# Performance work log

Hardware: AMD Instinct MI355X
Metric: run time of the kernel (lower is better)

## Reference

```python
import jax, jax.numpy as jnp
import numpy as np

N_NODES = 10000
N_EDGES = 320000
D_IN = 128
D_HID = 256
D_OUT = 128


def setup_inputs() -> dict:
    key = jax.random.key(0)
    k = jax.random.split(key, 6)
    idx_i = jax.random.randint(k[0], (N_EDGES,), 0, N_NODES)
    idx_j = jax.random.randint(k[1], (N_EDGES,), 0, N_NODES)
    prop = jax.random.normal(k[2], (N_NODES, D_IN), dtype=jnp.float32)
    basis = jax.random.normal(k[3], (N_EDGES, D_IN), dtype=jnp.float32)
    W1 = jax.random.normal(k[4], (D_IN, D_HID), dtype=jnp.float32) * (1.0 / np.sqrt(D_IN))
    b1 = jnp.zeros((D_HID,), dtype=jnp.float32)
    W2 = jax.random.normal(k[5], (D_HID, D_OUT), dtype=jnp.float32) * (1.0 / np.sqrt(D_HID))
    b2 = jnp.zeros((D_OUT,), dtype=jnp.float32)
    return {"idx_i": idx_i, "idx_j": idx_j, "prop": prop, "basis": basis,
            "W1": W1, "b1": b1, "W2": W2, "b2": b2}


def reference(idx_i, idx_j, prop, basis, W1, b1, W2, b2):
    # gather node features to edges, combine with basis: [E, D_IN]
    inter = prop[idx_i] + basis + prop[idx_j]
    # MLP: Linear(128->256) + tanh, then Linear(256->128) (no final activation)
    h = jnp.tanh(inter @ W1 + b1)  # [E, D_HID]
    out = h @ W2 + b2              # [E, D_OUT]
    return out
```

## Files before the change

kernel.cpp:

```cpp
#include <hip/hip_runtime.h>


#define N_EDGES 320000
#define DI 128
#define DH 256
#define DO 128
#define TM 64

typedef _Float16 half8v __attribute__((ext_vector_type(8)));
typedef _Float16 half4v __attribute__((ext_vector_type(4)));
typedef float floatx16 __attribute__((ext_vector_type(16)));

__device__ __forceinline__ float fast_tanh(float x) {
    float ax = __builtin_fabsf(x);
    float e = __expf(2.0f * ax);
    float t = 1.0f - 2.0f * __builtin_amdgcn_rcpf(e + 1.0f);
    return __builtin_copysignf(t, x);
}

__global__ __launch_bounds__(256) void wconvert(
    const float* __restrict__ W1, const float* __restrict__ W2,
    _Float16* __restrict__ W1T, _Float16* __restrict__ W2T)
{
    __shared__ float sT[32][33];
    int b = blockIdx.x;
    const float* src; _Float16* dst; int R, C, r0, c0;
    if (b < 32) { src = W1; dst = W1T; R = DI;  C = DH; r0 = (b & 3) * 32;  c0 = (b >> 2) * 32; }
    else { b -= 32; src = W2; dst = W2T; R = DH; C = DO; r0 = (b & 7) * 32; c0 = (b >> 3) * 32; }

    const int tid = threadIdx.x;
    const int cc = tid & 31, rr = tid >> 5;
    #pragma unroll
    for (int p = 0; p < 4; ++p) {
        int r = rr + p * 8;
        sT[r][cc] = src[(size_t)(r0 + r) * C + c0 + cc];
    }
    __syncthreads();
    #pragma unroll
    for (int p = 0; p < 4; ++p) {
        int c = rr + p * 8;
        dst[(size_t)(c0 + c) * R + r0 + cc] = (_Float16)sT[cc][c];
    }
}

__global__ __launch_bounds__(256) void pilayer_main(
    const int* __restrict__ idx_i, const int* __restrict__ idx_j,
    const float* __restrict__ prop, const float* __restrict__ basis,
    const _Float16* __restrict__ W1T, const float* __restrict__ b1,
    const _Float16* __restrict__ W2T, const float* __restrict__ b2,
    float* __restrict__ out)
{
    __shared__ _Float16 sA[TM][DI + 8];
    __shared__ _Float16 sH[TM][DH + 8];

    const int tid = threadIdx.x;
    const int e0 = blockIdx.x * TM;

    {
        const int c4 = (tid & 31) * 4;
        const int r0 = tid >> 5;
        #pragma unroll
        for (int p = 0; p < 8; ++p) {
            const int r = r0 + p * 8;
            const int e = e0 + r;
            const int ii = idx_i[e], jj = idx_j[e];
            const float4 a = *(const float4*)(prop  + (size_t)ii * DI + c4);
            const float4 bv = *(const float4*)(prop + (size_t)jj * DI + c4);
            const float4 c = *(const float4*)(basis + (size_t)e  * DI + c4);
            half4v hv;
            hv[0] = (_Float16)(a.x + bv.x + c.x);
            hv[1] = (_Float16)(a.y + bv.y + c.y);
            hv[2] = (_Float16)(a.z + bv.z + c.z);
            hv[3] = (_Float16)(a.w + bv.w + c.w);
            *(half4v*)(&sA[r][c4]) = hv;
        }
    }
    __syncthreads();

    const int w  = tid >> 6;
    const int l  = tid & 63;
    const int lm = l & 31;
    const int lk = (l >> 5) * 8;
    const int rowq = 4 * (l >> 5);

    floatx16 hacc[2][2] = {};
    {
        const _Float16* w1p = W1T + (size_t)(w * 64 + lm) * DI + lk;
        #pragma unroll 4
        for (int kt = 0; kt < 8; ++kt) {
            const int ko = kt * 16;
            half8v a0 = *(const half8v*)(&sA[lm][ko + lk]);
            half8v a1 = *(const half8v*)(&sA[32 + lm][ko + lk]);
            half8v b0 = *(const half8v*)(w1p + ko);
            half8v b1f = *(const half8v*)(w1p + 32 * DI + ko);
            hacc[0][0] = __builtin_amdgcn_mfma_f32_32x32x16_f16(a0, b0,  hacc[0][0], 0, 0, 0);
            hacc[1][0] = __builtin_amdgcn_mfma_f32_32x32x16_f16(a1, b0,  hacc[1][0], 0, 0, 0);
            hacc[0][1] = __builtin_amdgcn_mfma_f32_32x32x16_f16(a0, b1f, hacc[0][1], 0, 0, 0);
            hacc[1][1] = __builtin_amdgcn_mfma_f32_32x32x16_f16(a1, b1f, hacc[1][1], 0, 0, 0);
        }
    }

    {
        const float bias0 = b1[w * 64 + lm];
        const float bias1 = b1[w * 64 + 32 + lm];
        #pragma unroll
        for (int mt = 0; mt < 2; ++mt) {
            #pragma unroll
            for (int r = 0; r < 16; ++r) {
                const int row = mt * 32 + (r & 3) + 8 * (r >> 2) + rowq;
                sH[row][w * 64 + lm]      = (_Float16)fast_tanh(hacc[mt][0][r] + bias0);
                sH[row][w * 64 + 32 + lm] = (_Float16)fast_tanh(hacc[mt][1][r] + bias1);
            }
        }
    }
    __syncthreads();

    floatx16 oacc[2] = {};
    {
        const _Float16* w2p = W2T + (size_t)(w * 32 + lm) * DH + lk;
        #pragma unroll 4
        for (int kt = 0; kt < 16; ++kt) {
            const int ko = kt * 16;
            half8v a0 = *(const half8v*)(&sH[lm][ko + lk]);
            half8v a1 = *(const half8v*)(&sH[32 + lm][ko + lk]);
            half8v bb = *(const half8v*)(w2p + ko);
            oacc[0] = __builtin_amdgcn_mfma_f32_32x32x16_f16(a0, bb, oacc[0], 0, 0, 0);
            oacc[1] = __builtin_amdgcn_mfma_f32_32x32x16_f16(a1, bb, oacc[1], 0, 0, 0);
        }
    }

    {
        const int col = w * 32 + lm;
        const float bias = b2[col];
        #pragma unroll
        for (int mt = 0; mt < 2; ++mt) {
            #pragma unroll
            for (int r = 0; r < 16; ++r) {
                const int row = e0 + mt * 32 + (r & 3) + 8 * (r >> 2) + rowq;
                out[(size_t)row * DO + col] = oacc[mt][r] + bias;
            }
        }
    }
}

extern "C" void kernel_launch(void* const* d_in, const int* in_sizes, int n_in,
                              void* d_out, int out_size, void* d_ws, size_t ws_size,
                              hipStream_t stream) {
    const int*   idx_i = (const int*)d_in[0];
    const int*   idx_j = (const int*)d_in[1];
    const float* prop  = (const float*)d_in[2];
    const float* basis = (const float*)d_in[3];
    const float* W1    = (const float*)d_in[4];
    const float* b1    = (const float*)d_in[5];
    const float* W2    = (const float*)d_in[6];
    const float* b2    = (const float*)d_in[7];
    float* out = (float*)d_out;

    _Float16* W1T = (_Float16*)d_ws;
    _Float16* W2T = W1T + (size_t)DI * DH;

    wconvert<<<64, 256, 0, stream>>>(W1, W2, W1T, W2T);
    pilayer_main<<<N_EDGES / TM, 256, 0, stream>>>(idx_i, idx_j, prop, basis,
                                                   W1T, b1, W2T, b2, out);
}
```

Measured before the change: 379.7 us.

## Halve edge tile, alias sA/sH shared memory, and simplify tanh

Shrinks the per-block edge tile from 64 to 32 rows, so each wave does one M-tile of MFMAs and holds fewer accumulators. sA and sH now share one shared-memory buffer, separated by an extra barrier. A minimum-occupancy launch bound is added to get more resident blocks and better hide the latency of the gathers. tanh is computed with exp2 and no abs/copysign, which is cheaper but may overflow to inf for large inputs (it still saturates correctly). The cost is that each block reloads the weights for half as many edges, doubling weight-load traffic per edge.

```diff
diff --git a/kernel.cpp b/kernel.cpp
--- a/kernel.cpp
+++ b/kernel.cpp
@@ -5,17 +5,15 @@
 #define DI 128
 #define DH 256
 #define DO 128
-#define TM 64
+#define TM 32
 
 typedef _Float16 half8v __attribute__((ext_vector_type(8)));
 typedef _Float16 half4v __attribute__((ext_vector_type(4)));
 typedef float floatx16 __attribute__((ext_vector_type(16)));
 
 __device__ __forceinline__ float fast_tanh(float x) {
-    float ax = __builtin_fabsf(x);
-    float e = __expf(2.0f * ax);
-    float t = 1.0f - 2.0f * __builtin_amdgcn_rcpf(e + 1.0f);
-    return __builtin_copysignf(t, x);
+    float e = __builtin_amdgcn_exp2f(x * 2.885390081777927f);
+    return 1.0f - 2.0f * __builtin_amdgcn_rcpf(e + 1.0f);
 }
 
 __global__ __launch_bounds__(256) void wconvert(
@@ -43,15 +41,20 @@
     }
 }
 
-__global__ __launch_bounds__(256) void pilayer_main(
+#define SA_STRIDE (DI + 8)
+#define SH_STRIDE (DH + 8)
+#define SMEM_BYTES (TM * SH_STRIDE * 2)
+
+__global__ __launch_bounds__(256, 6) void pilayer_main(
     const int* __restrict__ idx_i, const int* __restrict__ idx_j,
     const float* __restrict__ prop, const float* __restrict__ basis,
     const _Float16* __restrict__ W1T, const float* __restrict__ b1,
     const _Float16* __restrict__ W2T, const float* __restrict__ b2,
     float* __restrict__ out)
 {
-    __shared__ _Float16 sA[TM][DI + 8];
-    __shared__ _Float16 sH[TM][DH + 8];
+    __shared__ char smem[SMEM_BYTES];
+    _Float16 (*sA)[SA_STRIDE] = (_Float16 (*)[SA_STRIDE])smem;
+    _Float16 (*sH)[SH_STRIDE] = (_Float16 (*)[SH_STRIDE])smem;
 
     const int tid = threadIdx.x;
     const int e0 = blockIdx.x * TM;
@@ -60,7 +63,7 @@
         const int c4 = (tid & 31) * 4;
         const int r0 = tid >> 5;
         #pragma unroll
-        for (int p = 0; p < 8; ++p) {
+        for (int p = 0; p < 4; ++p) {
             const int r = r0 + p * 8;
             const int e = e0 + r;
             const int ii = idx_i[e], jj = idx_j[e];
@@ -83,49 +86,42 @@
     const int lk = (l >> 5) * 8;
     const int rowq = 4 * (l >> 5);
 
-    floatx16 hacc[2][2] = {};
+    floatx16 hacc[2] = {};
     {
         const _Float16* w1p = W1T + (size_t)(w * 64 + lm) * DI + lk;
-        #pragma unroll 4
+        #pragma unroll 2
         for (int kt = 0; kt < 8; ++kt) {
             const int ko = kt * 16;
             half8v a0 = *(const half8v*)(&sA[lm][ko + lk]);
-            half8v a1 = *(const half8v*)(&sA[32 + lm][ko + lk]);
             half8v b0 = *(const half8v*)(w1p + ko);
             half8v b1f = *(const half8v*)(w1p + 32 * DI + ko);
-            hacc[0][0] = __builtin_amdgcn_mfma_f32_32x32x16_f16(a0, b0,  hacc[0][0], 0, 0, 0);
-            hacc[1][0] = __builtin_amdgcn_mfma_f32_32x32x16_f16(a1, b0,  hacc[1][0], 0, 0, 0);
-            hacc[0][1] = __builtin_amdgcn_mfma_f32_32x32x16_f16(a0, b1f, hacc[0][1], 0, 0, 0);
-            hacc[1][1] = __builtin_amdgcn_mfma_f32_32x32x16_f16(a1, b1f, hacc[1][1], 0, 0, 0);
+            hacc[0] = __builtin_amdgcn_mfma_f32_32x32x16_f16(a0, b0,  hacc[0], 0, 0, 0);
+            hacc[1] = __builtin_amdgcn_mfma_f32_32x32x16_f16(a0, b1f, hacc[1], 0, 0, 0);
         }
     }
+    __syncthreads();
 
     {
         const float bias0 = b1[w * 64 + lm];
         const float bias1 = b1[w * 64 + 32 + lm];
         #pragma unroll
-        for (int mt = 0; mt < 2; ++mt) {
-            #pragma unroll
-            for (int r = 0; r < 16; ++r) {
-                const int row = mt * 32 + (r & 3) + 8 * (r >> 2) + rowq;
-                sH[row][w * 64 + lm]      = (_Float16)fast_tanh(hacc[mt][0][r] + bias0);
-                sH[row][w * 64 + 32 + lm] = (_Float16)fast_tanh(hacc[mt][1][r] + bias1);
-            }
+        for (int r = 0; r < 16; ++r) {
+            const int row = (r & 3) + 8 * (r >> 2) + rowq;
+            sH[row][w * 64 + lm]      = (_Float16)fast_tanh(hacc[0][r] + bias0);
+            sH[row][w * 64 + 32 + lm] = (_Float16)fast_tanh(hacc[1][r] + bias1);
         }
     }
     __syncthreads();
 
-    floatx16 oacc[2] = {};
+    floatx16 oacc = {};
     {
         const _Float16* w2p = W2T + (size_t)(w * 32 + lm) * DH + lk;
-        #pragma unroll 4
+        #pragma unroll 2
         for (int kt = 0; kt < 16; ++kt) {
             const int ko = kt * 16;
             half8v a0 = *(const half8v*)(&sH[lm][ko + lk]);
-            half8v a1 = *(const half8v*)(&sH[32 + lm][ko + lk]);
             half8v bb = *(const half8v*)(w2p + ko);
-            oacc[0] = __builtin_amdgcn_mfma_f32_32x32x16_f16(a0, bb, oacc[0], 0, 0, 0);
-            oacc[1] = __builtin_amdgcn_mfma_f32_32x32x16_f16(a1, bb, oacc[1], 0, 0, 0);
+            oacc = __builtin_amdgcn_mfma_f32_32x32x16_f16(a0, bb, oacc, 0, 0, 0);
         }
     }
 
@@ -133,12 +129,9 @@
         const int col = w * 32 + lm;
         const float bias = b2[col];
         #pragma unroll
-        for (int mt = 0; mt < 2; ++mt) {
-            #pragma unroll
-            for (int r = 0; r < 16; ++r) {
-                const int row = e0 + mt * 32 + (r & 3) + 8 * (r >> 2) + rowq;
-                out[(size_t)row * DO + col] = oacc[mt][r] + bias;
-            }
+        for (int r = 0; r < 16; ++r) {
+            const int row = e0 + (r & 3) + 8 * (r >> 2) + rowq;
+            out[(size_t)row * DO + col] = oacc[r] + bias;
         }
     }
 }
```

Measured after the change: 447.3 us. 17.8% more time.
